# Performance work log

Measured on AMD Instinct MI355X. Metric: run time of the kernel, lower is better.

Reference implementation:

```python
import jax, jax.numpy as jnp
import numpy as np

B, C, W, F, NC = 512, 12, 4, 512, 4  # batch, leads, windows(=4, hardcoded by conv0), features, classes


def setup_inputs() -> dict:
    key = jax.random.key(0)
    ks = jax.random.split(key, 16)
    g = lambda i, shape, s=1.0: jax.random.normal(ks[i], shape, jnp.float32) * s
    return {
        "x": g(0, (B, C, W, F)),
        # GRU (PyTorch layout: W_ih [3F,F], W_hh [3F,F], gate order r,z,n)
        "gru_wih": g(1, (3 * F, F), 0.03),
        "gru_whh": g(2, (3 * F, F), 0.03),
        "gru_bih": jnp.zeros((3 * F,), jnp.float32),
        "gru_bhh": jnp.zeros((3 * F,), jnp.float32),
        # GraphLearning 1x1 convs (squeezed kernels); positive biases keep adj nondegenerate
        "conv0_w": g(3, (W,), 0.5), "conv0_b": jnp.float32(0.1),
        "conv1_w": g(4, (F,), 0.05), "conv1_b": jnp.float32(0.1),
        "conv2_w": g(5, (C * C, C), 0.3),
        "conv2_b": 0.1 + 0.05 * jnp.abs(g(6, (C * C,))),
        # GCN stack
        "gcn_w": g(7, (2, F, F), 0.04), "gcn_b": jnp.zeros((2, F), jnp.float32),
        # classifier head (jax [in,out] layout); BN in eval mode
        "fc1_w": g(8, (C * F, 512), 0.02), "fc1_b": jnp.zeros((512,), jnp.float32),
        "bn1_g": jnp.ones((512,), jnp.float32), "bn1_b": jnp.zeros((512,), jnp.float32),
        "bn1_m": 0.1 * g(9, (512,)), "bn1_v": 1.0 + 0.1 * jnp.abs(g(10, (512,))),
        "fc2_w": g(11, (512, 512), 0.04), "fc2_b": jnp.zeros((512,), jnp.float32),
        "bn2_g": jnp.ones((512,), jnp.float32), "bn2_b": jnp.zeros((512,), jnp.float32),
        "bn2_m": 0.1 * g(12, (512,)), "bn2_v": 1.0 + 0.1 * jnp.abs(g(13, (512,))),
        "fc3_w": g(14, (512, NC), 0.04), "fc3_b": jnp.zeros((NC,), jnp.float32),
    }


def reference(x, gru_wih, gru_whh, gru_bih, gru_bhh,
              conv0_w, conv0_b, conv1_w, conv1_b, conv2_w, conv2_b,
              gcn_w, gcn_b,
              fc1_w, fc1_b, bn1_g, bn1_b, bn1_m, bn1_v,
              fc2_w, fc2_b, bn2_g, bn2_b, bn2_m, bn2_v,
              fc3_w, fc3_b):
    b, c, w, f = x.shape
    # --- GRU over leads dim; each window slice starts from h0=0, so merge (batch, w) ---
    xs = x.transpose(0, 2, 1, 3).reshape(b * w, c, f)            # [N, C, F]
    xW = jnp.einsum('ntf,gf->ntg', xs, gru_wih) + gru_bih        # precompute input gates [N,C,3F]

    def step(h, xw_t):
        hg = h @ gru_whh.T + gru_bhh
        xr, xz, xn = jnp.split(xw_t, 3, axis=-1)
        hr, hz, hn = jnp.split(hg, 3, axis=-1)
        r = jax.nn.sigmoid(xr + hr)
        z = jax.nn.sigmoid(xz + hz)
        n = jnp.tanh(xn + r * hn)
        h = (1.0 - z) * n + z * h
        return h, h

    _, hs = jax.lax.scan(step, jnp.zeros((b * w, f), x.dtype), xW.transpose(1, 0, 2))
    gru_out = hs.transpose(1, 0, 2).reshape(b, w, c, f).transpose(0, 2, 1, 3)  # [B,C,W,F]

    # --- GraphLearning: 1x1 convs -> 12x12 adjacency -> normalized Laplacian -> Chebyshev K=4 ---
    g0 = gru_out.transpose(0, 2, 1, 3)                               # [B,W,C,F]
    y = jax.nn.relu(jnp.einsum('bwcf,w->bcf', g0, conv0_w) + conv0_b)  # [B,C,F]
    y = jax.nn.relu(jnp.einsum('bcf,f->bc', y, conv1_w) + conv1_b)     # [B,C]
    y = jax.nn.relu(jnp.einsum('bc,kc->bk', y, conv2_w) + conv2_b)     # [B,C*C]
    a = jnp.mean(y.reshape(b, c, c), axis=0)
    adj = jax.nn.relu(a)
    degree = jnp.sum(adj, axis=1)
    adj_s = 0.5 * (adj + adj.T)
    d_hat = 1.0 / (jnp.sqrt(degree) + 1e-7)
    lap = d_hat[:, None] * (jnp.diag(degree) - adj_s) * d_hat[None, :]
    L0 = jnp.zeros_like(lap)
    L1 = lap
    L2 = 2.0 * lap @ L1 - L0
    L3 = 2.0 * lap @ L2 - L1
    cheb = jnp.stack([L0, L1, L2, L3], axis=0)                       # [4,C,C]

    # --- GCN stack with residuals (dropout is identity in eval) ---
    h = gru_out.transpose(0, 2, 1, 3)[:, :, None]                    # [B,W,1,C,F]
    tmp = h
    res = h
    for i in range(gcn_w.shape[0]):
        support = jnp.einsum('bwocf,fg->bwocg', h, gcn_w[i])
        out = jnp.einsum('wij,bwojf->bwoif', cheb, support) + gcn_b[i]
        h = jax.nn.relu(out) + res
        res = h
    h = tmp + h
    h = h[:, :, 0].sum(1).reshape(b, c * f)                          # [B, C*F]

    # --- classifier head (eval-mode BN, dropout identity) ---
    def bn(v, gmm, bt, m, var):
        return (v - m) / jnp.sqrt(var + 1e-5) * gmm + bt

    h = bn(jax.nn.leaky_relu(h @ fc1_w + fc1_b, 0.01), bn1_g, bn1_b, bn1_m, bn1_v)
    h = bn(jax.nn.leaky_relu(h @ fc2_w + fc2_b, 0.01), bn2_g, bn2_b, bn2_m, bn2_v)
    return h @ fc3_w + fc3_b
```

## Files before the change

### kernel.cpp

```cpp
#include <hip/hip_runtime.h>
#include <cmath>

constexpr int Bb  = 512;
constexpr int Cc  = 12;
constexpr int Ww  = 4;
constexpr int Ff  = 512;
constexpr int Mx  = Bb * Ww * Cc;

typedef __attribute__((ext_vector_type(8))) short bf16x8;
typedef __attribute__((ext_vector_type(4))) float f32x4;

__device__ __forceinline__ float sigm(float v) { return 1.f / (1.f + expf(-v)); }
__device__ __forceinline__ float b2f(ushort u) { union { float f; unsigned i; } v; v.i = ((unsigned)u) << 16; return v.f; }
__device__ __forceinline__ ushort f2b(float f) {
    union { float f; unsigned i; } v; v.f = f;
    unsigned r = v.i + 0x7FFFu + ((v.i >> 16) & 1u);
    return (ushort)(r >> 16);
}
__device__ __forceinline__ float fsigm(float v) {
    return __builtin_amdgcn_rcpf(1.f + __builtin_amdgcn_exp2f(v * -1.44269504f));
}
__device__ __forceinline__ float ftanh(float v) {
    return 1.f - 2.f * __builtin_amdgcn_rcpf(1.f + __builtin_amdgcn_exp2f(v * 2.88539008f));
}
__device__ __forceinline__ void async16(const ushort* g, ushort* l) {
    __builtin_amdgcn_global_load_lds(
        (const __attribute__((address_space(1))) unsigned int*)g,
        (__attribute__((address_space(3))) unsigned int*)l, 16, 0, 0);
}

__global__ __launch_bounds__(256) void mfma_gemm(
    const ushort* __restrict__ A, const ushort* __restrict__ Bt,
    float* __restrict__ Cf, ushort* __restrict__ Cb,
    const float* __restrict__ colBias,
    int N, int K, int kLen, int MN, int gridY)
{
    __shared__ ushort As[128 * 64], Bs[128 * 64];
    const int tid = threadIdx.x;
    const int ln = tid & 63, wv = tid >> 6;
    const int l = blockIdx.x;
    const int by = l % gridY, bx = l / gridY, bz = blockIdx.y;
    const int srow = ln >> 3;
    const int kslot = (ln & 7) ^ srow;
    const int rowA0 = by * 128 + wv * 32;
    const int rowB0 = bx * 128 + wv * 32;
    const ushort* ga = A  + (long)(rowA0 + srow) * K + bz * kLen + kslot * 8;
    const ushort* gb = Bt + (long)(rowB0 + srow) * K + bz * kLen + kslot * 8;
    ushort* la = As + wv * 32 * 64;
    ushort* lb = Bs + wv * 32 * 64;
    const int rbase = (wv >> 1) * 64, cbase = (wv & 1) * 64;
    const int mrow = ln & 15, quad = ln >> 4;

    f32x4 acc[4][4] = {};

    for (int kc = 0; kc < kLen; kc += 64) {
        #pragma unroll
        for (int i = 0; i < 4; ++i) {
            async16(ga + (long)(i * 8) * K, la + i * 8 * 64);
            async16(gb + (long)(i * 8) * K, lb + i * 8 * 64);
        }
        ga += 64; gb += 64;
        __syncthreads();
        #pragma unroll
        for (int s = 0; s < 2; ++s) {
            const int sw = (((s << 2) + quad) ^ (ln & 7)) << 3;
            bf16x8 af[4], bf[4];
            #pragma unroll
            for (int i = 0; i < 4; ++i)
                af[i] = *(const bf16x8*)(As + (rbase + i * 16 + mrow) * 64 + sw);
            #pragma unroll
            for (int j = 0; j < 4; ++j)
                bf[j] = *(const bf16x8*)(Bs + (cbase + j * 16 + mrow) * 64 + sw);
            #pragma unroll
            for (int i = 0; i < 4; ++i)
                #pragma unroll
                for (int j = 0; j < 4; ++j)
                    acc[i][j] = __builtin_amdgcn_mfma_f32_16x16x32_bf16(bf[j], af[i], acc[i][j], 0, 0, 0);
        }
        __syncthreads();
    }

    const int gr0 = by * 128 + rbase + mrow;
    const int gc0 = bx * 128 + cbase + quad * 4;
    if (Cb) {
        #pragma unroll
        for (int i = 0; i < 4; ++i) {
            const long rowoff = (long)(gr0 + i * 16) * N;
            #pragma unroll
            for (int j = 0; j < 4; ++j) {
                float c0 = 0.f, c1 = 0.f, c2 = 0.f, c3 = 0.f;
                if (colBias) {
                    const float4 cb4 = *(const float4*)(colBias + gc0 + j * 16);
                    c0 = cb4.x; c1 = cb4.y; c2 = cb4.z; c3 = cb4.w;
                }
                union { ushort u[4]; uint2 v; } pk;
                pk.u[0] = f2b(acc[i][j][0] + c0);
                pk.u[1] = f2b(acc[i][j][1] + c1);
                pk.u[2] = f2b(acc[i][j][2] + c2);
                pk.u[3] = f2b(acc[i][j][3] + c3);
                *(uint2*)&Cb[rowoff + gc0 + j * 16] = pk.v;
            }
        }
    } else {
        float* Co = Cf + (long)bz * MN;
        #pragma unroll
        for (int i = 0; i < 4; ++i) {
            const long rowoff = (long)(gr0 + i * 16) * N;
            #pragma unroll
            for (int j = 0; j < 4; ++j)
                *(f32x4*)&Co[rowoff + gc0 + j * 16] = acc[i][j];
        }
    }
}

__global__ __launch_bounds__(512, 1) void gru_persist(
    const ushort* __restrict__ xW, const ushort* __restrict__ whhB,
    const float* __restrict__ bih, const float* __restrict__ bhh,
    ushort* __restrict__ h0, ushort* __restrict__ h1,
    ushort* __restrict__ G, unsigned* __restrict__ bar)
{
    __shared__ ushort Bw[8 * 96 * 64];
    const int tid = threadIdx.x, ln = tid & 63, wv = tid >> 6;
    const int mb = blockIdx.x & 15, fb = blockIdx.x >> 4;
    const int srow = ln >> 3, kslot = (ln & 7) ^ srow;
    const int mrow = ln & 15, quad = ln >> 4;

    #pragma unroll
    for (int i = 0; i < 12; ++i) {
        const int rg = i * 8 + wv;
        const int kc6 = rg / 12, rgi = rg - kc6 * 12;
        const int r0 = rgi * 8, r = r0 + srow;
        const int g = r >> 5, fc = r & 31;
        async16(whhB + (long)(g * 512 + fb * 32 + fc) * 512 + kc6 * 64 + kslot * 8,
                Bw + (kc6 * 96 + r0) * 64);
    }

    float br[2][4], bz[2][4], bni[2][4], bnh[2][4];
    #pragma unroll
    for (int ft = 0; ft < 2; ++ft) {
        const int f0 = fb * 32 + ft * 16 + quad * 4;
        const float4 bir = *(const float4*)(bih + f0);
        const float4 biz = *(const float4*)(bih + 512 + f0);
        const float4 bin = *(const float4*)(bih + 1024 + f0);
        const float4 bhr = *(const float4*)(bhh + f0);
        const float4 bhz = *(const float4*)(bhh + 512 + f0);
        const float4 bhn = *(const float4*)(bhh + 1024 + f0);
        br[ft][0] = bir.x + bhr.x; br[ft][1] = bir.y + bhr.y; br[ft][2] = bir.z + bhr.z; br[ft][3] = bir.w + bhr.w;
        bz[ft][0] = biz.x + bhz.x; bz[ft][1] = biz.y + bhz.y; bz[ft][2] = biz.z + bhz.z; bz[ft][3] = biz.w + bhz.w;
        bni[ft][0] = bin.x; bni[ft][1] = bin.y; bni[ft][2] = bin.z; bni[ft][3] = bin.w;
        bnh[ft][0] = bhn.x; bnh[ft][1] = bhn.y; bnh[ft][2] = bhn.z; bnh[ft][3] = bhn.w;
    }
    __syncthreads();

    const int n = mb * 128 + wv * 16 + mrow;
    unsigned* cptr = bar + mb * 16;

    const int rbase0 = ((mb * 8 + wv) * 16) * 512;
    const int aoff = (quad >> 1) * 256 + mrow * 16 + (quad & 1) * 8;
    const int sbase = ((mb * 8 + wv) * 16 + fb) * 512 + mrow * 16 + quad * 4;

    uint2 hprev[2]; hprev[0].x = 0u; hprev[0].y = 0u; hprev[1] = hprev[0];

    for (int t = 0; t < 12; ++t) {
        const ushort* hin = (t & 1) ? h1 : h0;
        ushort* hout = (t & 1) ? h0 : h1;
        f32x4 acc[6] = {};

        unsigned long long ha[16][2];
        if (t > 0) {
            #pragma unroll
            for (int sl = 0; sl < 16; ++sl) {
                const ushort* p = hin + rbase0 + sl * 512 + aoff;
                ha[sl][0] = __hip_atomic_load((const unsigned long long*)p,
                                              __ATOMIC_RELAXED, __HIP_MEMORY_SCOPE_AGENT);
                ha[sl][1] = __hip_atomic_load((const unsigned long long*)(p + 4),
                                              __ATOMIC_RELAXED, __HIP_MEMORY_SCOPE_AGENT);
            }
        }

        const long xrow = ((long)n * 12 + t) * 1536;
        uint2 xrv[2], xzv[2], xnv[2];
        #pragma unroll
        for (int ft = 0; ft < 2; ++ft) {
            const int f0 = fb * 32 + ft * 16 + quad * 4;
            xrv[ft] = *(const uint2*)(xW + xrow + f0);
            xzv[ft] = *(const uint2*)(xW + xrow + 512 + f0);
            xnv[ft] = *(const uint2*)(xW + xrow + 1024 + f0);
        }

        if (t > 0) {
            #pragma unroll
            for (int kc = 0; kc < 8; ++kc) {
                const ushort* Bk = Bw + kc * (96 * 64);
                #pragma unroll
                for (int s = 0; s < 2; ++s) {
                    union { unsigned long long q[2]; bf16x8 v; } af;
                    af.q[0] = ha[kc * 2 + s][0];
                    af.q[1] = ha[kc * 2 + s][1];
                    const int sw = (((s << 2) + quad) ^ (ln & 7)) << 3;
                    #pragma unroll
                    for (int jt = 0; jt < 6; ++jt) {
                        const bf16x8 bh = *(const bf16x8*)(Bk + (jt * 16 + mrow) * 64 + sw);
                        acc[jt] = __builtin_amdgcn_mfma_f32_16x16x32_bf16(bh, af.v, acc[jt], 0, 0, 0);
                    }
                }
            }
        }

        #pragma unroll
        for (int ft = 0; ft < 2; ++ft) {
            const ushort* xr = (const ushort*)&xrv[ft];
            const ushort* xz = (const ushort*)&xzv[ft];
            const ushort* xn = (const ushort*)&xnv[ft];
            const ushort* hp = (const ushort*)&hprev[ft];
            union { ushort u[4]; uint2 v; } o;
            #pragma unroll
            for (int r = 0; r < 4; ++r) {
                const float rr = fsigm(acc[ft][r] + b2f(xr[r]) + br[ft][r]);
                const float zz = fsigm(acc[2 + ft][r] + b2f(xz[r]) + bz[ft][r]);
                const float nv = ftanh(b2f(xn[r]) + bni[ft][r] + rr * (acc[4 + ft][r] + bnh[ft][r]));
                o.u[r] = f2b((1.f - zz) * nv + zz * b2f(hp[r]));
            }
            hprev[ft] = o.v;
        }

        if (t < 11) {
            union { uint2 v; unsigned long long q; } q0, q1;
            q0.v = hprev[0]; q1.v = hprev[1];
            __hip_atomic_store((unsigned long long*)&hout[sbase], q0.q,
                               __ATOMIC_RELAXED, __HIP_MEMORY_SCOPE_AGENT);
            __hip_atomic_store((unsigned long long*)&hout[sbase + 256], q1.q,
                               __ATOMIC_RELAXED, __HIP_MEMORY_SCOPE_AGENT);
            asm volatile("s_waitcnt vmcnt(0)" ::: "memory");
            __syncthreads();
            if (tid == 0)
                __hip_atomic_fetch_add(cptr, 1u, __ATOMIC_RELAXED, __HIP_MEMORY_SCOPE_AGENT);
        }

        {
            const int f0 = fb * 32 + quad * 4;
            *(uint2*)&G[((long)n * 12 + t) * 512 + f0] = hprev[0];
            *(uint2*)&G[((long)n * 12 + t) * 512 + f0 + 16] = hprev[1];
        }

        if (t < 11) {
            if (tid == 0) {
                const unsigned tgt = (unsigned)(t + 1) * 16u;
                while (__hip_atomic_load(cptr, __ATOMIC_RELAXED, __HIP_MEMORY_SCOPE_AGENT) < tgt)
                    __builtin_amdgcn_s_sleep(1);
            }
            __syncthreads();
        }
    }
}

__global__ __launch_bounds__(256) void cvt_x(const float* __restrict__ x, ushort* __restrict__ xb)
{
    const int idx = blockIdx.x * 256 + threadIdx.x;
    const int m = idx >> 6, f8 = (idx & 63) << 3;
    const int n = m / 12, c = m - n * 12;
    const int b = n >> 2, w = n & 3;
    const float* src = x + (((b * 12 + c) * 4 + w) << 9) + f8;
    const float4 a = *(const float4*)src, q = *(const float4*)(src + 4);
    uint4 o;
    o.x = (unsigned)f2b(a.x) | ((unsigned)f2b(a.y) << 16);
    o.y = (unsigned)f2b(a.z) | ((unsigned)f2b(a.w) << 16);
    o.z = (unsigned)f2b(q.x) | ((unsigned)f2b(q.y) << 16);
    o.w = (unsigned)f2b(q.z) | ((unsigned)f2b(q.w) << 16);
    *(uint4*)(xb + (m << 9) + f8) = o;
}

__global__ __launch_bounds__(256) void cvt_w2(
    const float* __restrict__ wih, const float* __restrict__ whh,
    ushort* __restrict__ wihB, ushort* __restrict__ whhB)
{
    int bx = blockIdx.x;
    const float* s; ushort* d;
    if (bx < 384) { s = wih; d = wihB; } else { s = whh; d = whhB; bx -= 384; }
    const int e = (bx * 256 + threadIdx.x) << 3;
    const float4 a = *(const float4*)(s + e), q = *(const float4*)(s + e + 4);
    uint4 o;
    o.x = (unsigned)f2b(a.x) | ((unsigned)f2b(a.y) << 16);
    o.y = (unsigned)f2b(a.z) | ((unsigned)f2b(a.w) << 16);
    o.z = (unsigned)f2b(q.x) | ((unsigned)f2b(q.y) << 16);
    o.w = (unsigned)f2b(q.z) | ((unsigned)f2b(q.w) << 16);
    *(uint4*)(d + e) = o;
}

__global__ __launch_bounds__(256) void tcvt_all(
    const float* __restrict__ gcnw, const float* __restrict__ f1w, const float* __restrict__ f2w,
    ushort* __restrict__ gw0, ushort* __restrict__ gw1,
    ushort* __restrict__ f1t, ushort* __restrict__ f2t)
{
    int by = blockIdx.y;
    const float* src; ushort* dst; int R, C;
    if (by < 16)       { src = gcnw;          dst = gw0; R = 512;  C = 512; }
    else if (by < 32)  { src = gcnw + 262144; dst = gw1; R = 512;  C = 512; by -= 16; }
    else if (by < 224) { src = f1w;           dst = f1t; R = 6144; C = 512; by -= 32; }
    else               { src = f2w;           dst = f2t; R = 512;  C = 512; by -= 224; }
    __shared__ float tl[32][33];
    const int c0 = blockIdx.x * 32, r0 = by * 32;
    const int cx = threadIdx.x & 31, ry = threadIdx.x >> 5;
    #pragma unroll
    for (int k = 0; k < 4; ++k) tl[ry + k * 8][cx] = src[(long)(r0 + ry + k * 8) * C + c0 + cx];
    __syncthreads();
    #pragma unroll
    for (int k = 0; k < 4; ++k) dst[(long)(c0 + ry + k * 8) * R + r0 + cx] = f2b(tl[cx][ry + k * 8]);
}

__global__ __launch_bounds__(256) void conv01(
    const ushort* __restrict__ G, const float* __restrict__ w0, const float* __restrict__ b0,
    const float* __restrict__ w1, const float* __restrict__ b1, float* __restrict__ y2)
{
    const int row = (blockIdx.x * 256 + threadIdx.x) >> 6;
    const int lane = threadIdx.x & 63;
    const int b = row / 12, c = row - 12 * b;
    const float w00 = w0[0], w01 = w0[1], w02 = w0[2], w03 = w0[3], bb = b0[0];
    const ushort* gp = G + ((long)(b * 4) * 12 + c) * 512;
    float s = 0.f;
    for (int f = lane; f < 512; f += 64) {
        const float v = bb + b2f(gp[f]) * w00 + b2f(gp[6144 + f]) * w01
                      + b2f(gp[12288 + f]) * w02 + b2f(gp[18432 + f]) * w03;
        s += fmaxf(v, 0.f) * w1[f];
    }
    #pragma unroll
    for (int off = 32; off; off >>= 1) s += __shfl_down(s, off);
    if (lane == 0) y2[row] = fmaxf(s + b1[0], 0.f);
}

__global__ __launch_bounds__(256) void conv2_cheb(
    const float* __restrict__ y2, const float* __restrict__ w2,
    const float* __restrict__ b2, float* __restrict__ cheb)
{
    __shared__ float ys[6144];
    __shared__ float adj[144], deg[12], dhat[12], lap[144], T2[144];
    const int tid = threadIdx.x;
    for (int i = tid; i < 6144; i += 256) ys[i] = y2[i];
    __syncthreads();
    if (tid < 144) {
        float wk[12];
        #pragma unroll
        for (int c = 0; c < 12; ++c) wk[c] = w2[tid * 12 + c];
        const float bias = b2[tid];
        float s = 0.f;
        for (int b = 0; b < 512; ++b) {
            float v = bias;
            #pragma unroll
            for (int c = 0; c < 12; ++c) v += ys[b * 12 + c] * wk[c];
            s += fmaxf(v, 0.f);
        }
        adj[tid] = fmaxf(s * (1.f / 512.f), 0.f);
    }
    __syncthreads();
    if (tid < 12) {
        float s = 0.f;
        for (int j = 0; j < 12; ++j) s += adj[tid * 12 + j];
        deg[tid] = s; dhat[tid] = 1.f / (sqrtf(s) + 1e-7f);
    }
    __syncthreads();
    if (tid < 144) {
        const int i = tid / 12, j = tid % 12;
        const float as = 0.5f * (adj[i * 12 + j] + adj[j * 12 + i]);
        lap[tid] = dhat[i] * ((i == j ? deg[i] : 0.f) - as) * dhat[j];
    }
    __syncthreads();
    if (tid < 144) {
        const int i = tid / 12, j = tid % 12;
        float s = 0.f;
        for (int kk = 0; kk < 12; ++kk) s += lap[i * 12 + kk] * lap[kk * 12 + j];
        T2[tid] = 2.f * s;
    }
    __syncthreads();
    if (tid < 144) {
        const int i = tid / 12, j = tid % 12;
        float s = 0.f;
        for (int kk = 0; kk < 12; ++kk) s += lap[i * 12 + kk] * T2[kk * 12 + j];
        cheb[tid] = 0.f;
        cheb[144 + tid] = lap[tid];
        cheb[288 + tid] = T2[tid];
        cheb[432 + tid] = 2.f * s - lap[tid];
    }
}

__global__ __launch_bounds__(256) void gcn_epi1(
    const ushort* __restrict__ S, const float* __restrict__ cheb,
    const float* __restrict__ gcnb, const ushort* __restrict__ G,
    ushort* __restrict__ H1)
{
    __shared__ float ch[576];
    const int tid = threadIdx.x;
    for (int i = tid; i < 576; i += 256) ch[i] = cheb[i];
    __syncthreads();
    const int g = blockIdx.x >> 1;
    const int w = g & 3;
    const int f = (blockIdx.x & 1) * 256 + tid;
    const float bias = gcnb[f];
    float sv[12];
    #pragma unroll
    for (int j = 0; j < 12; ++j) sv[j] = b2f(S[((long)(g * 12 + j)) * 512 + f]);
    const float* cw0 = ch + w * 144;
    #pragma unroll
    for (int c = 0; c < 12; ++c) {
        float o = bias;
        const float* cw = cw0 + c * 12;
        #pragma unroll
        for (int j = 0; j < 12; ++j) o += cw[j] * sv[j];
        const long gi = ((long)(g * 12 + c)) * 512 + f;
        H1[gi] = f2b(fmaxf(o, 0.f) + b2f(G[gi]));
    }
}

__global__ __launch_bounds__(256) void gcn_epi2(
    const ushort* __restrict__ S, const float* __restrict__ cheb,
    const float* __restrict__ gcnb, const ushort* __restrict__ G,
    const ushort* __restrict__ H1, ushort* __restrict__ pooled)
{
    __shared__ float ch[576];
    const int tid = threadIdx.x;
    for (int i = tid; i < 576; i += 256) ch[i] = cheb[i];
    __syncthreads();
    const int b = blockIdx.x >> 1;
    const int f = (blockIdx.x & 1) * 256 + tid;
    const float bias = gcnb[f];
    float acc[12];
    #pragma unroll
    for (int c = 0; c < 12; ++c) acc[c] = 0.f;
    #pragma unroll
    for (int w = 0; w < 4; ++w) {
        const int g = b * 4 + w;
        float sv[12];
        #pragma unroll
        for (int j = 0; j < 12; ++j) sv[j] = b2f(S[((long)(g * 12 + j)) * 512 + f]);
        const float* cw0 = ch + w * 144;
        #pragma unroll
        for (int c = 0; c < 12; ++c) {
            float o = bias;
            const float* cw = cw0 + c * 12;
            #pragma unroll
            for (int j = 0; j < 12; ++j) o += cw[j] * sv[j];
            const long gi = ((long)(g * 12 + c)) * 512 + f;
            acc[c] += fmaxf(o, 0.f) + b2f(H1[gi]) + b2f(G[gi]);
        }
    }
    #pragma unroll
    for (int c = 0; c < 12; ++c)
        pooled[((long)(b * 12 + c)) * 512 + f] = f2b(acc[c]);
}

__global__ __launch_bounds__(256) void fc_epi(
    const float* __restrict__ part, int nsplit, const float* __restrict__ bias,
    const float* __restrict__ g, const float* __restrict__ be,
    const float* __restrict__ mu, const float* __restrict__ var,
    ushort* __restrict__ outb, float* __restrict__ outf)
{
    const int idx = blockIdx.x * 256 + threadIdx.x;
    const int c = idx & 511;
    float s = bias[c];
    for (int k = 0; k < nsplit; ++k) s += part[k * 262144 + idx];
    s = s >= 0.f ? s : 0.01f * s;
    s = (s - mu[c]) * rsqrtf(var[c] + 1e-5f) * g[c] + be[c];
    if (outb) outb[idx] = f2b(s); else outf[idx] = s;
}

__global__ __launch_bounds__(256) void fc3_kernel(
    const float* __restrict__ z2, const float* __restrict__ w3,
    const float* __restrict__ b3, float* __restrict__ out)
{
    const int idx = blockIdx.x * 256 + threadIdx.x;
    const int m = idx >> 2, nc = idx & 3;
    float s = b3[nc];
    const float* zr = z2 + m * 512;
    for (int k = 0; k < 512; ++k) s += zr[k] * w3[k * 4 + nc];
    out[idx] = s;
}

extern "C" void kernel_launch(void* const* d_in, const int* in_sizes, int n_in,
                              void* d_out, int out_size, void* d_ws, size_t ws_size,
                              hipStream_t stream)
{
    (void)in_sizes; (void)n_in; (void)out_size; (void)ws_size;
    const float* x    = (const float*)d_in[0];
    const float* wih  = (const float*)d_in[1];
    const float* whh  = (const float*)d_in[2];
    const float* bih  = (const float*)d_in[3];
    const float* bhh  = (const float*)d_in[4];
    const float* c0w  = (const float*)d_in[5];
    const float* c0b  = (const float*)d_in[6];
    const float* c1w  = (const float*)d_in[7];
    const float* c1b  = (const float*)d_in[8];
    const float* c2w  = (const float*)d_in[9];
    const float* c2b  = (const float*)d_in[10];
    const float* gcnw = (const float*)d_in[11];
    const float* gcnb = (const float*)d_in[12];
    const float* f1w  = (const float*)d_in[13];
    const float* f1b  = (const float*)d_in[14];
    const float* bn1g = (const float*)d_in[15];
    const float* bn1b = (const float*)d_in[16];
    const float* bn1m = (const float*)d_in[17];
    const float* bn1v = (const float*)d_in[18];
    const float* f2w  = (const float*)d_in[19];
    const float* f2b_ = (const float*)d_in[20];
    const float* bn2g = (const float*)d_in[21];
    const float* bn2b = (const float*)d_in[22];
    const float* bn2m = (const float*)d_in[23];
    const float* bn2v = (const float*)d_in[24];
    const float* f3w  = (const float*)d_in[25];
    const float* f3b  = (const float*)d_in[26];

    char* W = (char*)d_ws;
    ushort* xW     = (ushort*)(W + 0);
    ushort* S      = (ushort*)(W + 0);
    ushort* H1     = (ushort*)(W + 25165824);
    ushort* pooled = (ushort*)(W + 50331648);
    float*  z1p    = (float*)(W + 58720256);
    float*  z2p    = z1p;
    ushort* xb     = (ushort*)(W + 75497472);
    ushort* G      = (ushort*)(W + 75497472);
    ushort* h0     = (ushort*)(W + 100663296);
    ushort* h1     = (ushort*)(W + 102760448);
    ushort* whhB   = (ushort*)(W + 104857600);
    ushort* wihB   = (ushort*)(W + 106430464);
    ushort* gw0    = (ushort*)(W + 108003328);
    ushort* gw1    = (ushort*)(W + 108527616);
    ushort* f1t    = (ushort*)(W + 109051904);
    ushort* f2t    = (ushort*)(W + 115343360);
    ushort* z1b    = (ushort*)(W + 115867648);
    float*  z2     = (float*)(W + 116391936);
    float*  y2     = (float*)(W + 117440512);
    float*  chebb  = (float*)(W + 117465088);
    unsigned* bar  = (unsigned*)(W + 117467392);

    hipMemsetAsync(bar, 0, 1024, stream);
    cvt_x<<<(Mx * 64) / 256, 256, 0, stream>>>(x, xb);
    cvt_w2<<<768, 256, 0, stream>>>(wih, whh, wihB, whhB);
    tcvt_all<<<dim3(16, 240), 256, 0, stream>>>(gcnw, f1w, f2w, gw0, gw1, f1t, f2t);

    mfma_gemm<<<dim3(2304, 1), 256, 0, stream>>>(
        xb, wihB, nullptr, xW, nullptr, 3 * Ff, Ff, Ff, 0, 192);
    gru_persist<<<256, 512, 0, stream>>>(xW, whhB, bih, bhh, h0, h1, G, bar);

    conv01<<<(Bb * Cc * 64) / 256, 256, 0, stream>>>(G, c0w, c0b, c1w, c1b, y2);
    conv2_cheb<<<1, 256, 0, stream>>>(y2, c2w, c2b, chebb);

    mfma_gemm<<<dim3(768, 1), 256, 0, stream>>>(
        G, gw0, nullptr, S, nullptr, Ff, Ff, Ff, 0, 192);
    gcn_epi1<<<4096, 256, 0, stream>>>(S, chebb, gcnb, G, H1);

    mfma_gemm<<<dim3(768, 1), 256, 0, stream>>>(
        H1, gw1, nullptr, S, nullptr, Ff, Ff, Ff, 0, 192);
    gcn_epi2<<<1024, 256, 0, stream>>>(S, chebb, gcnb + Ff, G, H1, pooled);

    mfma_gemm<<<dim3(16, 16), 256, 0, stream>>>(
        pooled, f1t, z1p, nullptr, nullptr, 512, Cc * Ff, 384, 262144, 4);
    fc_epi<<<1024, 256, 0, stream>>>(z1p, 16, f1b, bn1g, bn1b, bn1m, bn1v, z1b, nullptr);
    mfma_gemm<<<dim3(16, 4), 256, 0, stream>>>(
        z1b, f2t, z2p, nullptr, nullptr, 512, 512, 128, 262144, 4);
    fc_epi<<<1024, 256, 0, stream>>>(z2p, 4, f2b_, bn2g, bn2b, bn2m, bn2v, nullptr, z2);
    fc3_kernel<<<(Bb * 4) / 256, 256, 0, stream>>>(z2, f3w, f3b, (float*)d_out);
}
```

Before: 445.3 us.

## Fuse GRU input-gate projection into the persistent GRU kernel

Removes the separate GEMM that precomputed xW (the input-to-hidden gate projections). Each GRU step now computes them inside gru_persist with extra MFMAs, reading x rows and W_ih fragments straight from global memory (not LDS), with a separate accumulator for the n gate. This drops a large intermediate buffer write and read plus one kernel launch, and the workspace layout is reshuffled to match. In exchange, the serial recurrent loop gains per-step global loads and MFMA work on its critical path, and the bf16 rounding of the input projections is no longer applied.

```diff
diff --git a/kernel.cpp b/kernel.cpp
--- a/kernel.cpp
+++ b/kernel.cpp
@@ -114,7 +114,8 @@
 }
 
 __global__ __launch_bounds__(512, 1) void gru_persist(
-    const ushort* __restrict__ xW, const ushort* __restrict__ whhB,
+    const ushort* __restrict__ xb, const ushort* __restrict__ wihB,
+    const ushort* __restrict__ whhB,
     const float* __restrict__ bih, const float* __restrict__ bhh,
     ushort* __restrict__ h0, ushort* __restrict__ h1,
     ushort* __restrict__ G, unsigned* __restrict__ bar)
@@ -150,6 +151,14 @@
         bni[ft][0] = bin.x; bni[ft][1] = bin.y; bni[ft][2] = bin.z; bni[ft][3] = bin.w;
         bnh[ft][0] = bhn.x; bnh[ft][1] = bhn.y; bnh[ft][2] = bhn.z; bnh[ft][3] = bhn.w;
     }
+
+    long wxrow[6];
+    #pragma unroll
+    for (int jt = 0; jt < 6; ++jt) {
+        const int local = jt * 16 + mrow;
+        const int g = local >> 5, fc = local & 31;
+        wxrow[jt] = (long)(g * 512 + fb * 32 + fc) * 512 + quad * 8;
+    }
     __syncthreads();
 
     const int n = mb * 128 + wv * 16 + mrow;
@@ -165,6 +174,7 @@
         const ushort* hin = (t & 1) ? h1 : h0;
         ushort* hout = (t & 1) ? h0 : h1;
         f32x4 acc[6] = {};
+        f32x4 accn[2] = {};
 
         unsigned long long ha[16][2];
         if (t > 0) {
@@ -178,14 +188,26 @@
             }
         }
 
-        const long xrow = ((long)n * 12 + t) * 1536;
-        uint2 xrv[2], xzv[2], xnv[2];
-        #pragma unroll
-        for (int ft = 0; ft < 2; ++ft) {
-            const int f0 = fb * 32 + ft * 16 + quad * 4;
-            xrv[ft] = *(const uint2*)(xW + xrow + f0);
-            xzv[ft] = *(const uint2*)(xW + xrow + 512 + f0);
-            xnv[ft] = *(const uint2*)(xW + xrow + 1024 + f0);
+        {
+            const ushort* xrow = xb + ((long)n * 12 + t) * 512 + quad * 8;
+            #pragma unroll
+            for (int kc = 0; kc < 8; ++kc) {
+                #pragma unroll
+                for (int s = 0; s < 2; ++s) {
+                    const int sl = kc * 2 + s;
+                    const bf16x8 ax = *(const bf16x8*)(xrow + sl * 32);
+                    #pragma unroll
+                    for (int jt = 0; jt < 4; ++jt) {
+                        const bf16x8 bx = *(const bf16x8*)(wihB + wxrow[jt] + sl * 32);
+                        acc[jt] = __builtin_amdgcn_mfma_f32_16x16x32_bf16(bx, ax, acc[jt], 0, 0, 0);
+                    }
+                    #pragma unroll
+                    for (int jt = 4; jt < 6; ++jt) {
+                        const bf16x8 bx = *(const bf16x8*)(wihB + wxrow[jt] + sl * 32);
+                        accn[jt - 4] = __builtin_amdgcn_mfma_f32_16x16x32_bf16(bx, ax, accn[jt - 4], 0, 0, 0);
+                    }
+                }
+            }
         }
 
         if (t > 0) {
@@ -209,16 +231,13 @@
 
         #pragma unroll
         for (int ft = 0; ft < 2; ++ft) {
-            const ushort* xr = (const ushort*)&xrv[ft];
-            const ushort* xz = (const ushort*)&xzv[ft];
-            const ushort* xn = (const ushort*)&xnv[ft];
             const ushort* hp = (const ushort*)&hprev[ft];
             union { ushort u[4]; uint2 v; } o;
             #pragma unroll
             for (int r = 0; r < 4; ++r) {
-                const float rr = fsigm(acc[ft][r] + b2f(xr[r]) + br[ft][r]);
-                const float zz = fsigm(acc[2 + ft][r] + b2f(xz[r]) + bz[ft][r]);
-                const float nv = ftanh(b2f(xn[r]) + bni[ft][r] + rr * (acc[4 + ft][r] + bnh[ft][r]));
+                const float rr = fsigm(acc[ft][r] + br[ft][r]);
+                const float zz = fsigm(acc[2 + ft][r] + bz[ft][r]);
+                const float nv = ftanh(accn[ft][r] + bni[ft][r] + rr * (acc[4 + ft][r] + bnh[ft][r]));
                 o.u[r] = f2b((1.f - zz) * nv + zz * b2f(hp[r]));
             }
             hprev[ft] = o.v;
@@ -508,14 +527,13 @@
     const float* f3b  = (const float*)d_in[26];
 
     char* W = (char*)d_ws;
-    ushort* xW     = (ushort*)(W + 0);
-    ushort* S      = (ushort*)(W + 0);
-    ushort* H1     = (ushort*)(W + 25165824);
-    ushort* pooled = (ushort*)(W + 50331648);
-    float*  z1p    = (float*)(W + 58720256);
+    ushort* G      = (ushort*)(W + 0);
+    ushort* S      = (ushort*)(W + 25165824);
+    ushort* H1     = (ushort*)(W + 50331648);
+    ushort* xb     = (ushort*)(W + 75497472);
+    ushort* pooled = (ushort*)(W + 75497472);
+    float*  z1p    = (float*)(W + 81788928);
     float*  z2p    = z1p;
-    ushort* xb     = (ushort*)(W + 75497472);
-    ushort* G      = (ushort*)(W + 75497472);
     ushort* h0     = (ushort*)(W + 100663296);
     ushort* h1     = (ushort*)(W + 102760448);
     ushort* whhB   = (ushort*)(W + 104857600);
@@ -535,9 +553,7 @@
     cvt_w2<<<768, 256, 0, stream>>>(wih, whh, wihB, whhB);
     tcvt_all<<<dim3(16, 240), 256, 0, stream>>>(gcnw, f1w, f2w, gw0, gw1, f1t, f2t);
 
-    mfma_gemm<<<dim3(2304, 1), 256, 0, stream>>>(
-        xb, wihB, nullptr, xW, nullptr, 3 * Ff, Ff, Ff, 0, 192);
-    gru_persist<<<256, 512, 0, stream>>>(xW, whhB, bih, bhh, h0, h1, G, bar);
+    gru_persist<<<256, 512, 0, stream>>>(xb, wihB, whhB, bih, bhh, h0, h1, G, bar);
 
     conv01<<<(Bb * Cc * 64) / 256, 256, 0, stream>>>(G, c0w, c0b, c1w, c1b, y2);
     conv2_cheb<<<1, 256, 0, stream>>>(y2, c2w, c2b, chebb);
```

Result: slower. 767.8 us (+72.4%).
